# Kernel optimization log

Hardware: AMD Instinct MI355X
Metric: run time of the kernel (lower is better)

The kernel has to match this reference:

```python
import jax, jax.numpy as jnp
import numpy as np

RADIUS = 3       # corr_radius
NUM_LEVELS = 4   # corr_lvls


def avg_pool2(x):
    """2x2 avg-pool with stride 2 on the last two axes (floor semantics, like F.avg_pool2d)."""
    nd = x.ndim
    s = jax.lax.reduce_window(
        x, 0.0, jax.lax.add,
        window_dimensions=(1,) * (nd - 2) + (2, 2),
        window_strides=(1,) * (nd - 2) + (2, 2),
        padding='VALID')
    return s * 0.25


def bilinear_window_lookup(corr, coords, radius):
    """corr: [B,H,W,hl,wl] per-pixel correlation maps; coords: [B,H,W,2] (x,y) in
    level-pixel units. Samples a (2r+1)^2 window around each coord with bilinear
    interpolation and zero padding (matches grid_sample align_corners=True, zeros).
    Returns [B,H,W,(2r+1)^2]."""
    B, H, W, hl, wl = corr.shape
    r = radius
    d = jnp.arange(-r, r + 1, dtype=coords.dtype)
    dy, dx = jnp.meshgrid(d, d, indexing='ij')
    delta = jnp.stack([dx.ravel(), dy.ravel()], axis=-1)        # [K2,2] (x,y)
    pts = coords[:, :, :, None, :] + delta                       # [B,H,W,K2,2]
    x, y = pts[..., 0], pts[..., 1]
    x0 = jnp.floor(x); y0 = jnp.floor(y)
    x1 = x0 + 1.0;     y1 = y0 + 1.0
    wx1 = x - x0; wx0 = 1.0 - wx1
    wy1 = y - y0; wy0 = 1.0 - wy1
    bi = jnp.arange(B)[:, None, None, None]
    hi = jnp.arange(H)[None, :, None, None]
    wi = jnp.arange(W)[None, None, :, None]

    def gather(xc, yc):
        valid = (xc >= 0) & (xc <= wl - 1) & (yc >= 0) & (yc <= hl - 1)
        xi = jnp.clip(xc, 0, wl - 1).astype(jnp.int32)
        yi = jnp.clip(yc, 0, hl - 1).astype(jnp.int32)
        return corr[bi, hi, wi, yi, xi] * valid.astype(corr.dtype)

    return (gather(x0, y0) * wx0 * wy0 + gather(x1, y0) * wx1 * wy0 +
            gather(x0, y1) * wx0 * wy1 + gather(x1, y1) * wx1 * wy1)


def pyramid_lookup(pyr, coords, radius):
    """pyr: list of [B,H,W,hl,wl]; coords: [B,H,W,2] at full level-0 resolution.
    Returns [B, L*(2r+1)^2, H, W]."""
    outs = [bilinear_window_lookup(c, coords / float(2 ** lvl), radius)
            for lvl, c in enumerate(pyr)]
    out = jnp.concatenate(outs, axis=-1)
    return jnp.transpose(out, (0, 3, 1, 2))


def setup_inputs() -> dict:
    key = jax.random.key(0)
    k0, k1, k2, k3, k4 = jax.random.split(key, 5)
    B, D, H, W = 1, 128, 60, 108  # 1/8-res features of a padded 480x864 frame
    fmap0 = jax.random.normal(k0, (B, D, H, W), dtype=jnp.float32)
    fmap1 = jax.random.normal(k1, (B, D, H, W), dtype=jnp.float32)
    flow0 = jax.random.normal(k2, (B, 2, H, W), dtype=jnp.float32)
    flow1 = jax.random.normal(k3, (B, 2, H, W), dtype=jnp.float32)
    embt = jax.random.uniform(k4, (B, 1, 1, 1), dtype=jnp.float32,
                              minval=0.1, maxval=0.9)
    return {"fmap0": fmap0, "fmap1": fmap1, "flow0": flow0,
            "flow1": flow1, "embt": embt}


def reference(fmap0, fmap1, flow0, flow1, embt):
    """BidirCorrBlock construction + AMT._corr_scale_lookup (downsample=1).
    Returns [B, 2*L*(2r+1)^2 + 4, H, W]: bidirectional multi-level correlation
    features concatenated with the stacked flows (corr, flow of the torch code)."""
    B, D, H, W = fmap0.shape
    # all-pairs correlation volume, scaled by 1/sqrt(D) as in RAFT's CorrBlock
    corr = jnp.einsum('bchw,bcuv->bhwuv', fmap0, fmap1) / jnp.sqrt(
        jnp.asarray(D, fmap0.dtype))                       # [B,H,W,H,W]
    corr_T = jnp.transpose(corr, (0, 3, 4, 1, 2))          # reversed direction
    pyr, pyr_T = [corr], [corr_T]
    for _ in range(NUM_LEVELS - 1):
        pyr.append(avg_pool2(pyr[-1]))
        pyr_T.append(avg_pool2(pyr_T[-1]))

    # coords_grid: channels (x, y)
    ys, xs = jnp.meshgrid(jnp.arange(H, dtype=fmap0.dtype),
                          jnp.arange(W, dtype=fmap0.dtype), indexing='ij')
    coord = jnp.broadcast_to(jnp.stack([xs, ys], axis=-1), (B, H, W, 2))

    t1_scale = 1.0 / embt           # [B,1,1,1]
    t0_scale = 1.0 / (1.0 - embt)
    f0 = jnp.transpose(flow0, (0, 2, 3, 1))  # [B,H,W,2]
    f1 = jnp.transpose(flow1, (0, 2, 3, 1))
    coords0 = coord + f1 * t1_scale          # lookup args of corr_fn(...)
    coords1 = coord + f0 * t0_scale

    corr0 = pyramid_lookup(pyr, coords0, RADIUS)     # [B, L*K2, H, W]
    corr1 = pyramid_lookup(pyr_T, coords1, RADIUS)
    corr_out = jnp.concatenate([corr0, corr1], axis=1)
    flow_out = jnp.concatenate([flow0, flow1], axis=1)
    return jnp.concatenate([corr_out, flow_out], axis=1)
```

## Files before the change

### kernel.cpp

```cpp
#include <hip/hip_runtime.h>

typedef _Float16 h16;
typedef __attribute__((ext_vector_type(2))) h16 h2v;
typedef __attribute__((ext_vector_type(8))) h16 h8v;

constexpr int H_ = 60, W_ = 108, HW_ = 6480;

constexpr unsigned B_F0T  = 0;
constexpr unsigned B_F1T  = 1658880;
constexpr unsigned B_F0L1 = 3317760;
constexpr unsigned B_F0L2 = 3732480;
constexpr unsigned B_F0L3 = 3836160;
constexpr unsigned B_F1L1 = 3859456;
constexpr unsigned B_F1L2 = 4274176;
constexpr unsigned B_F1L3 = 4377856;

__global__ __launch_bounds__(256) void k_transpose(const float* __restrict__ f0,
                                                   const float* __restrict__ f1,
                                                   h16* __restrict__ ws) {
    __shared__ float lds[64 * 129];
    const float* src = blockIdx.y ? f1 : f0;
    h16* dst = (h16*)((char*)ws + (blockIdx.y ? B_F1T : B_F0T));
    const int p0 = blockIdx.x * 64;
    const int t  = threadIdx.x;
    const int pr = t & 63, cr = t >> 6;
    #pragma unroll
    for (int cb = 0; cb < 128; cb += 4) {
        int c = cb + cr, p = p0 + pr;
        if (p < HW_) lds[pr * 129 + c] = src[(size_t)c * HW_ + p];
    }
    __syncthreads();
    const int cw = t & 63, pw = t >> 6;
    #pragma unroll
    for (int pb = 0; pb < 64; pb += 4) {
        int p = p0 + pb + pw;
        if (p < HW_) {
            float a = lds[(pb + pw) * 129 + 2 * cw];
            float b = lds[(pb + pw) * 129 + 2 * cw + 1];
            h2v v; v.x = (h16)a; v.y = (h16)b;
            ((h2v*)dst)[(size_t)p * 64 + cw] = v;
        }
    }
}

__global__ __launch_bounds__(256) void k_pyramid(h16* __restrict__ wsh) {
    char* ws = (char*)wsh;
    const int map = blockIdx.y;
    const unsigned srcB = map ? B_F1T : B_F0T;
    const char* s = ws + srcB;
    const int bid = blockIdx.x;
    const int t = threadIdx.x;

    if (bid < 102) {
        const int idx = bid * 256 + t;
        if (idx >= 1620 * 16) return;
        const int pos = idx >> 4, q = idx & 15;
        const int y = pos / 54, x = pos - y * 54;
        const unsigned r0 = (unsigned)(2 * y * 108 + 2 * x) * 256 + q * 16;
        const unsigned r1 = r0 + 108 * 256;
        h8v a = *(const h8v*)(s + r0);
        h8v b = *(const h8v*)(s + r0 + 256);
        h8v c = *(const h8v*)(s + r1);
        h8v d = *(const h8v*)(s + r1 + 256);
        h8v o;
        #pragma unroll
        for (int k = 0; k < 8; ++k)
            o[k] = (h16)((((float)a[k] + (float)b[k]) + ((float)c[k] + (float)d[k])) * 0.25f);
        *(h8v*)(ws + (map ? B_F1L1 : B_F0L1) + (unsigned)pos * 256 + q * 16) = o;
    } else if (bid < 128) {
        const int idx = (bid - 102) * 256 + t;
        if (idx >= 405 * 16) return;
        const int pos = idx >> 4, q = idx & 15;
        const int y = pos / 27, x = pos - y * 27;
        float acc[8] = {};
        #pragma unroll
        for (int dy = 0; dy < 4; ++dy) {
            #pragma unroll
            for (int dx = 0; dx < 4; ++dx) {
                h8v u = *(const h8v*)(s + (unsigned)((4 * y + dy) * 108 + 4 * x + dx) * 256 + q * 16);
                #pragma unroll
                for (int k = 0; k < 8; ++k) acc[k] += (float)u[k];
            }
        }
        h8v o;
        #pragma unroll
        for (int k = 0; k < 8; ++k) o[k] = (h16)(acc[k] * 0.0625f);
        *(h8v*)(ws + (map ? B_F1L2 : B_F0L2) + (unsigned)pos * 256 + q * 16) = o;
    } else {
        const int idx = (bid - 128) * 256 + t;
        if (idx >= 91 * 128) return;
        const int pos = idx >> 7;
        const int sub = idx & 127;
        const int half = sub >> 6, lane = sub & 63;
        const int j = lane >> 3, qq = (lane & 7) + half * 8;
        const int y = pos / 13, x = pos - y * 13;
        float acc[8] = {};
        #pragma unroll
        for (int dx = 0; dx < 8; ++dx) {
            h8v u = *(const h8v*)(s + (unsigned)((8 * y + j) * 108 + 8 * x + dx) * 256 + qq * 16);
            #pragma unroll
            for (int k = 0; k < 8; ++k) acc[k] += (float)u[k];
        }
        #pragma unroll
        for (int k = 0; k < 8; ++k) {
            acc[k] += __shfl_xor(acc[k], 8);
            acc[k] += __shfl_xor(acc[k], 16);
            acc[k] += __shfl_xor(acc[k], 32);
        }
        if (j == 0) {
            h8v o;
            #pragma unroll
            for (int k = 0; k < 8; ++k) o[k] = (h16)(acc[k] * 0.015625f);
            *(h8v*)(ws + (map ? B_F1L3 : B_F0L3) + (unsigned)pos * 256 + qq * 16) = o;
        }
    }
}

template <int CTRL>
__device__ __forceinline__ float dpp_add(float x) {
    int y = __builtin_amdgcn_update_dpp(0, __builtin_bit_cast(int, x),
                                        CTRL, 0xF, 0xF, true);
    return x + __builtin_bit_cast(float, y);
}

__device__ __forceinline__ float dot_u4(uint4 u, uint4 s, float acc) {
    acc = __builtin_amdgcn_fdot2(__builtin_bit_cast(h2v, u.x),
                                 __builtin_bit_cast(h2v, s.x), acc, false);
    acc = __builtin_amdgcn_fdot2(__builtin_bit_cast(h2v, u.y),
                                 __builtin_bit_cast(h2v, s.y), acc, false);
    acc = __builtin_amdgcn_fdot2(__builtin_bit_cast(h2v, u.z),
                                 __builtin_bit_cast(h2v, s.z), acc, false);
    acc = __builtin_amdgcn_fdot2(__builtin_bit_cast(h2v, u.w),
                                 __builtin_bit_cast(h2v, s.w), acc, false);
    return acc;
}

__global__ __launch_bounds__(256, 4) void k_lookup(const h16* __restrict__ wsh,
                                                   const float* __restrict__ flow0,
                                                   const float* __restrict__ flow1,
                                                   const float* __restrict__ embt,
                                                   float* __restrict__ out) {
    __shared__ float so[196][5];
    const char* ws = (const char*)wsh;
    const int bid = blockIdx.x;
    const int xcd = bid & 7;
    const int dir = xcd >> 2;
    const int ord = (xcd & 3) * 405 + (bid >> 3);
    const int pix0 = ord * 4;
    const int t = threadIdx.x;
    const int L = t & 63;
    const int pix = pix0 + (t >> 6);
    const int h = pix / 108, w = pix - h * 108;

    const float e = embt[0];
    const float scale = dir ? 1.0f / (1.0f - e) : 1.0f / e;
    const float* fl = dir ? flow0 : flow1;
    const float cx = (float)w + fl[pix] * scale;
    const float cy = (float)h + fl[HW_ + pix] * scale;

    const int ch = L & 7;
    const int p  = L >> 3;

    const unsigned sbase = (dir ? B_F1T : B_F0T) + (unsigned)pix * 256;
    uint4 su0 = *(const uint4*)(ws + sbase + ch * 16);
    uint4 su1 = *(const uint4*)(ws + sbase + 128 + ch * 16);
    {
        h8v a = __builtin_bit_cast(h8v, su0), b = __builtin_bit_cast(h8v, su1);
        #pragma unroll
        for (int k = 0; k < 8; ++k) {
            a[k] = a[k] * (h16)0.08838834764831845f;
            b[k] = b[k] * (h16)0.08838834764831845f;
        }
        su0 = __builtin_bit_cast(uint4, a);
        su1 = __builtin_bit_cast(uint4, b);
    }

    constexpr unsigned g0[4] = {B_F1T, B_F1L1, B_F1L2, B_F1L3};
    constexpr unsigned g1[4] = {B_F0T, B_F0L1, B_F0L2, B_F0L3};

    #pragma unroll
    for (int lvl = 0; lvl < 4; ++lvl) {
        const unsigned gbase = dir ? g1[lvl] : g0[lvl];
        const int wl = 108 >> lvl, hl = 60 >> lvl;
        const float inv = (lvl == 0) ? 1.f : (lvl == 1) ? 0.5f : (lvl == 2) ? 0.25f : 0.125f;
        const float cxl = cx * inv, cyl = cy * inv;
        const float bxf = floorf(cxl), byf = floorf(cyl);
        const int bx = (int)bxf, by = (int)byf;
        const int gx = bx - 3 + p;
        const int gxc = min(max(gx, 0), wl - 1);
        const bool colv = (gx >= 0) & (gx < wl);
        const int gyo = by - 3 + ch;
        const bool ownv = colv & (gyo >= 0) & (gyo < hl);

        const unsigned coloff = gbase + (unsigned)gxc * 256 + (unsigned)ch * 16;
        uint4 u0[8], u1[8];
        #pragma unroll
        for (int j = 0; j < 8; ++j) {
            const int gy = by - 3 + j;
            const int gyc = min(max(gy, 0), hl - 1);
            const unsigned ro = coloff + (unsigned)(gyc * wl) * 256;
            u0[j] = *(const uint4*)(ws + ro);
            u1[j] = *(const uint4*)(ws + ro + 128);
        }

        float dval = 0.0f;
        #pragma unroll
        for (int j = 0; j < 8; ++j) {
            float a0 = dot_u4(u0[j], su0, 0.0f);
            float a1 = dot_u4(u1[j], su1, 0.0f);
            float acc = a0 + a1;
            acc = dpp_add<0xB1>(acc);
            acc = dpp_add<0x4E>(acc);
            acc = dpp_add<0x141>(acc);
            dval = (ch == j) ? acc : dval;
        }
        dval = ownv ? dval : 0.0f;

        const int dyi = L / 7, dxi = L - dyi * 7;
        const float fx = cxl - bxf, fy = cyl - byf;
        const float d00 = __shfl(dval, 8 * dxi + dyi);
        const float d01 = __shfl(dval, 8 * dxi + dyi + 8);
        const float d10 = __shfl(dval, 8 * dxi + dyi + 1);
        const float d11 = __shfl(dval, 8 * dxi + dyi + 9);
        const float v = (d00 * (1.0f - fx) + d01 * fx) * (1.0f - fy) +
                        (d10 * (1.0f - fx) + d11 * fx) * fy;
        if (L < 49) so[lvl * 49 + L][t >> 6] = v;
    }
    __syncthreads();

    if (t < 196) {
        float4 o = make_float4(so[t][0], so[t][1], so[t][2], so[t][3]);
        *(float4*)(out + (size_t)(dir * 196 + t) * HW_ + pix0) = o;
    } else if (dir == 0 && t < 200) {
        const int c = t - 196;
        const float* f = (c < 2) ? flow0 + (size_t)c * HW_
                                 : flow1 + (size_t)(c - 2) * HW_;
        *(float4*)(out + (size_t)(392 + c) * HW_ + pix0) = *(const float4*)(f + pix0);
    }
}

extern "C" void kernel_launch(void* const* d_in, const int* in_sizes, int n_in,
                              void* d_out, int out_size, void* d_ws, size_t ws_size,
                              hipStream_t stream) {
    const float* fmap0 = (const float*)d_in[0];
    const float* fmap1 = (const float*)d_in[1];
    const float* flow0 = (const float*)d_in[2];
    const float* flow1 = (const float*)d_in[3];
    const float* embt  = (const float*)d_in[4];
    h16* ws  = (h16*)d_ws;
    float* out = (float*)d_out;

    k_transpose<<<dim3(102, 2), 256, 0, stream>>>(fmap0, fmap1, ws);
    k_pyramid<<<dim3(174, 2), 256, 0, stream>>>(ws);
    k_lookup<<<dim3(405 * 8), 256, 0, stream>>>(ws, flow0, flow1, embt, out);
}
```

Before: 44.62 us.

## Stage level-3 pyramid features in LDS and fold score scale into transpose

Each lookup block now copies the whole level-3 feature map (91 positions x 256 bytes) into shared memory and reads its level-3 window from LDS instead of global memory. The 1/sqrt(D) scaling is split as a sqrt factor applied to both feature maps during the transpose, which removes the per-thread fp16 multiply of the source vector in the lookup kernel. The cost is about 23 KB of extra LDS per block, which can lower occupancy, plus a preload and a __syncthreads in every block. The pyramid levels now hold pre-scaled features, which also changes fp16 rounding.

```diff
diff --git a/kernel.cpp b/kernel.cpp
--- a/kernel.cpp
+++ b/kernel.cpp
@@ -30,13 +30,14 @@
         if (p < HW_) lds[pr * 129 + c] = src[(size_t)c * HW_ + p];
     }
     __syncthreads();
+    const float S = 0.29730177875068026f;
     const int cw = t & 63, pw = t >> 6;
     #pragma unroll
     for (int pb = 0; pb < 64; pb += 4) {
         int p = p0 + pb + pw;
         if (p < HW_) {
-            float a = lds[(pb + pw) * 129 + 2 * cw];
-            float b = lds[(pb + pw) * 129 + 2 * cw + 1];
+            float a = lds[(pb + pw) * 129 + 2 * cw] * S;
+            float b = lds[(pb + pw) * 129 + 2 * cw + 1] * S;
             h2v v; v.x = (h16)a; v.y = (h16)b;
             ((h2v*)dst)[(size_t)p * 64 + cw] = v;
         }
@@ -46,8 +47,7 @@
 __global__ __launch_bounds__(256) void k_pyramid(h16* __restrict__ wsh) {
     char* ws = (char*)wsh;
     const int map = blockIdx.y;
-    const unsigned srcB = map ? B_F1T : B_F0T;
-    const char* s = ws + srcB;
+    const char* s = ws + (map ? B_F1T : B_F0T);
     const int bid = blockIdx.x;
     const int t = threadIdx.x;
 
@@ -141,6 +141,7 @@
                                                    const float* __restrict__ embt,
                                                    float* __restrict__ out) {
     __shared__ float so[196][5];
+    __shared__ char l3cache[91 * 256];
     const char* ws = (const char*)wsh;
     const int bid = blockIdx.x;
     const int xcd = bid & 7;
@@ -152,6 +153,16 @@
     const int pix = pix0 + (t >> 6);
     const int h = pix / 108, w = pix - h * 108;
 
+    {
+        const char* l3src = ws + (dir ? B_F0L3 : B_F1L3);
+        #pragma unroll
+        for (int i = 0; i < 6; ++i) {
+            const int c = t + i * 256;
+            if (c < 91 * 16)
+                ((uint4*)l3cache)[c] = *(const uint4*)(l3src + c * 16);
+        }
+    }
+
     const float e = embt[0];
     const float scale = dir ? 1.0f / (1.0f - e) : 1.0f / e;
     const float* fl = dir ? flow0 : flow1;
@@ -162,21 +173,13 @@
     const int p  = L >> 3;
 
     const unsigned sbase = (dir ? B_F1T : B_F0T) + (unsigned)pix * 256;
-    uint4 su0 = *(const uint4*)(ws + sbase + ch * 16);
-    uint4 su1 = *(const uint4*)(ws + sbase + 128 + ch * 16);
-    {
-        h8v a = __builtin_bit_cast(h8v, su0), b = __builtin_bit_cast(h8v, su1);
-        #pragma unroll
-        for (int k = 0; k < 8; ++k) {
-            a[k] = a[k] * (h16)0.08838834764831845f;
-            b[k] = b[k] * (h16)0.08838834764831845f;
-        }
-        su0 = __builtin_bit_cast(uint4, a);
-        su1 = __builtin_bit_cast(uint4, b);
-    }
+    const uint4 su0 = *(const uint4*)(ws + sbase + ch * 16);
+    const uint4 su1 = *(const uint4*)(ws + sbase + 128 + ch * 16);
 
     constexpr unsigned g0[4] = {B_F1T, B_F1L1, B_F1L2, B_F1L3};
     constexpr unsigned g1[4] = {B_F0T, B_F0L1, B_F0L2, B_F0L3};
+
+    __syncthreads();
 
     #pragma unroll
     for (int lvl = 0; lvl < 4; ++lvl) {
@@ -192,15 +195,27 @@
         const int gyo = by - 3 + ch;
         const bool ownv = colv & (gyo >= 0) & (gyo < hl);
 
-        const unsigned coloff = gbase + (unsigned)gxc * 256 + (unsigned)ch * 16;
         uint4 u0[8], u1[8];
-        #pragma unroll
-        for (int j = 0; j < 8; ++j) {
-            const int gy = by - 3 + j;
-            const int gyc = min(max(gy, 0), hl - 1);
-            const unsigned ro = coloff + (unsigned)(gyc * wl) * 256;
-            u0[j] = *(const uint4*)(ws + ro);
-            u1[j] = *(const uint4*)(ws + ro + 128);
+        if (lvl == 3) {
+            const unsigned co = (unsigned)gxc * 256 + (unsigned)ch * 16;
+            #pragma unroll
+            for (int j = 0; j < 8; ++j) {
+                const int gy = by - 3 + j;
+                const int gyc = min(max(gy, 0), hl - 1);
+                const unsigned ro = co + (unsigned)(gyc * wl) * 256;
+                u0[j] = *(const uint4*)(l3cache + ro);
+                u1[j] = *(const uint4*)(l3cache + ro + 128);
+            }
+        } else {
+            const unsigned coloff = gbase + (unsigned)gxc * 256 + (unsigned)ch * 16;
+            #pragma unroll
+            for (int j = 0; j < 8; ++j) {
+                const int gy = by - 3 + j;
+                const int gyc = min(max(gy, 0), hl - 1);
+                const unsigned ro = coloff + (unsigned)(gyc * wl) * 256;
+                u0[j] = *(const uint4*)(ws + ro);
+                u1[j] = *(const uint4*)(ws + ro + 128);
+            }
         }
 
         float dval = 0.0f;
```

New measurement: 42.06 us. -5.7%, faster.
